# Kernel optimization log

Hardware: AMD Instinct MI355X
Metric: run time of the kernel (lower is better)

## Reference

```python
import jax, jax.numpy as jnp
import numpy as np

N = 100000   # nodes
E = 1600000  # edges (avg degree 16)
F_IN, F_HID, F_OUT = 128, 64, 16


def setup_inputs() -> dict:
    key = jax.random.key(0)
    ks = jax.random.split(key, 8)
    x = jax.random.normal(ks[0], (N, F_IN), jnp.float32)
    edge_index = jax.random.randint(ks[1], (2, E), 0, N, dtype=jnp.int32)
    def glorot(k, fan_in, fan_out):
        return jax.random.normal(k, (fan_in, fan_out), jnp.float32) * (1.0 / np.sqrt(fan_in))
    return {
        "x": x,
        "edge_index": edge_index,
        "W1": glorot(ks[2], F_IN, F_HID), "b1": jnp.zeros((F_HID,), jnp.float32),
        "W2": glorot(ks[3], F_HID, F_HID), "b2": jnp.zeros((F_HID,), jnp.float32),
        "W3": glorot(ks[4], F_HID, F_HID), "b3": jnp.zeros((F_HID,), jnp.float32),
        "W4": glorot(ks[5], F_HID, F_OUT), "b4": jnp.zeros((F_OUT,), jnp.float32),
    }


def _gcn_norm(edge_index, num_nodes):
    # Add self-loops and compute symmetric normalization D^-1/2 (A+I) D^-1/2
    loop = jnp.arange(num_nodes, dtype=edge_index.dtype)
    src = jnp.concatenate([edge_index[0], loop])
    dst = jnp.concatenate([edge_index[1], loop])
    deg = jax.ops.segment_sum(jnp.ones_like(dst, jnp.float32), dst, num_segments=num_nodes)
    dinv = jnp.where(deg > 0, jax.lax.rsqrt(deg), 0.0)
    norm = dinv[src] * dinv[dst]  # [E+N]
    return src, dst, norm


def _gcn_conv(x, W, b, src, dst, norm, num_nodes):
    h = x @ W                       # [N, F_out] small GEMM first (PyG order)
    msg = h[src] * norm[:, None]    # [E+N, F_out] gather + scale
    out = jax.ops.segment_sum(msg, dst, num_segments=num_nodes)
    return out + b


def reference(x, edge_index, W1, b1, W2, b2, W3, b3, W4, b4):
    src, dst, norm = _gcn_norm(edge_index, N)
    h = jax.nn.relu(_gcn_conv(x, W1, b1, src, dst, norm, N))  # dropout is identity in eval
    h = jax.nn.relu(_gcn_conv(h, W2, b2, src, dst, norm, N))
    h = jax.nn.relu(_gcn_conv(h, W3, b3, src, dst, norm, N))
    return _gcn_conv(h, W4, b4, src, dst, norm, N)
```

## Files before the change

kernel.cpp:

```cpp
#include <hip/hip_runtime.h>
#include <hip/hip_bf16.h>
#include <stdint.h>


#define TPB 256
#define MAXDEG 64
#define NGRP 8
#define NBLK_P 256
#define SLABCAP 1536
#define OVCAP 65536

typedef unsigned int uint;
typedef _Float16 h8 __attribute__((ext_vector_type(8)));
typedef _Float16 h16 __attribute__((ext_vector_type(16)));
typedef float f4 __attribute__((ext_vector_type(4)));

__device__ __forceinline__ int swz(int f) {
    return ((f >> 3) & 3) * 16 + (f >> 5) * 8 + (f & 7);
}

__device__ __forceinline__ int grp_of(int d, int chunk, float invchunk) {
    int g = (int)((float)d * invchunk);
    if (d >= (g + 1) * chunk) ++g;
    else if (d < g * chunk) --g;
    return g;
}

__global__ __launch_bounds__(TPB) void k_part(const int* __restrict__ src,
                                              const int* __restrict__ dst,
                                              uint* __restrict__ pcount,
                                              uint* __restrict__ ovcnt,
                                              int* __restrict__ ovbuf,
                                              uint* __restrict__ slab,
                                              int E, int chunk, float invchunk,
                                              int range) {
    __shared__ uint lcnt[NGRP];
    if (threadIdx.x < NGRP) lcnt[threadIdx.x] = 0;
    __syncthreads();
    const int e0 = blockIdx.x * range;
    const int e1 = (e0 + range < E) ? e0 + range : E;
    for (int e = e0 + (int)threadIdx.x; e < e1; e += TPB) {
        int d = dst[e];
        int s = src[e];
        int g = grp_of(d, chunk, invchunk);
        uint pos = atomicAdd(&lcnt[g], 1u);
        uint val = ((uint)(d - g * chunk) << 17) | (uint)s;
        if (pos < SLABCAP) {
            slab[((size_t)blockIdx.x * NGRP + g) * SLABCAP + pos] = val;
        } else {
            uint p = atomicAdd(ovcnt, 1u);
            if (p < OVCAP) { ovbuf[2 * p] = d; ovbuf[2 * p + 1] = s; }
        }
    }
    __syncthreads();
    if (threadIdx.x < NGRP) {
        uint c = lcnt[threadIdx.x];
        pcount[blockIdx.x * NGRP + threadIdx.x] = (c < SLABCAP) ? c : SLABCAP;
    }
}

__global__ __launch_bounds__(TPB) void k_fill(const uint* __restrict__ slab,
                                              const uint* __restrict__ pcount,
                                              const uint* __restrict__ ovcnt,
                                              const int* __restrict__ ovbuf,
                                              uint* __restrict__ cnt,
                                              int* __restrict__ bucket,
                                              int chunk) {
    const int grp = blockIdx.x & (NGRP - 1);
    const int blk = blockIdx.x >> 3;
    const int n = (int)pcount[blk * NGRP + grp];
    const uint* s = slab + ((size_t)blk * NGRP + grp) * SLABCAP;
    const int dbase = grp * chunk;
    int e = (int)threadIdx.x;
    for (; e + TPB < n; e += 2 * TPB) {
        uint v0 = s[e];
        uint v1 = s[e + TPB];
        int d0 = dbase + (int)(v0 >> 17), s0 = (int)(v0 & 0x1FFFFu);
        int d1 = dbase + (int)(v1 >> 17), s1 = (int)(v1 & 0x1FFFFu);
        uint p0 = atomicAdd(&cnt[d0], 1u);
        uint p1 = atomicAdd(&cnt[d1], 1u);
        if (p0 < MAXDEG) bucket[(size_t)d0 * MAXDEG + (int)p0] = s0;
        if (p1 < MAXDEG) bucket[(size_t)d1 * MAXDEG + (int)p1] = s1;
    }
    if (e < n) {
        uint v = s[e];
        int d = dbase + (int)(v >> 17), sv = (int)(v & 0x1FFFFu);
        uint p = atomicAdd(&cnt[d], 1u);
        if (p < MAXDEG) bucket[(size_t)d * MAXDEG + (int)p] = sv;
    }
    if (blk == 0) {
        uint on = *ovcnt;
        if (on > OVCAP) on = OVCAP;
        for (uint i = threadIdx.x; i < on; i += TPB) {
            int d = ovbuf[2 * i];
            if (d >= dbase && d < dbase + chunk) {
                int sv = ovbuf[2 * i + 1];
                uint p = atomicAdd(&cnt[d], 1u);
                if (p < MAXDEG) bucket[(size_t)d * MAXDEG + (int)p] = sv;
            }
        }
    }
}

__global__ __launch_bounds__(TPB) void k_gemm_mfma128(const float* __restrict__ X,
                                                      const float* __restrict__ W,
                                                      const uint* __restrict__ cnt,
                                                      _Float16* __restrict__ H,
                                                      int ngrp16, int nwaves, int n) {
    const int lane = threadIdx.x & 63;
    const int wid = blockIdx.x * (TPB / 64) + (threadIdx.x >> 6);
    const int nrow = lane & 15;
    const int kgrp = lane >> 4;

    h8 Bf[4][4];
#pragma unroll
    for (int kb = 0; kb < 4; ++kb)
#pragma unroll
        for (int j = 0; j < 8; ++j) {
            int k = kb * 32 + kgrp * 8 + j;
#pragma unroll
            for (int cb = 0; cb < 4; ++cb)
                Bf[kb][cb][j] = (_Float16)W[k * 64 + cb * 16 + nrow];
        }

    for (int g = wid; g < ngrp16; g += nwaves) {
        const int base = g * 16;
        int arow = base + nrow; if (arow >= n) arow = n - 1;
        const float* xr = X + (size_t)arow * 128;
        h8 A[4];
#pragma unroll
        for (int kb = 0; kb < 4; ++kb) {
            f4 lo = *(const f4*)(xr + kb * 32 + kgrp * 8);
            f4 hi = *(const f4*)(xr + kb * 32 + kgrp * 8 + 4);
#pragma unroll
            for (int j = 0; j < 4; ++j) { A[kb][j] = (_Float16)lo[j]; A[kb][4 + j] = (_Float16)hi[j]; }
        }
        f4 D[4];
#pragma unroll
        for (int cb = 0; cb < 4; ++cb) {
            f4 d = {0.f, 0.f, 0.f, 0.f};
#pragma unroll
            for (int kb = 0; kb < 4; ++kb)
                d = __builtin_amdgcn_mfma_f32_16x16x32_f16(A[kb], Bf[kb][cb], d, 0, 0, 0);
            D[cb] = d;
        }
#pragma unroll
        for (int r = 0; r < 4; ++r) {
            int onode = base + kgrp * 4 + r;
            if (onode < n) {
                float dio = rsqrtf((float)cnt[onode] + 1.0f);
#pragma unroll
                for (int cb = 0; cb < 4; ++cb)
                    H[(size_t)onode * 64 + swz(cb * 16 + nrow)] = (_Float16)(D[cb][r] * dio);
            }
        }
    }
}

template <int FOUT>
__global__ __launch_bounds__(TPB, 2) void k_agg_mfma(const _Float16* __restrict__ H,
                                                     const int* __restrict__ bucket,
                                                     const uint* __restrict__ cnt,
                                                     const float* __restrict__ b,
                                                     const float* __restrict__ W,
                                                     _Float16* __restrict__ Hout,
                                                     int ngrp16, int nwaves) {
    const int lane = threadIdx.x & 63;
    const int wid = blockIdx.x * (TPB / 64) + (threadIdx.x >> 6);
    const int nrow = lane & 15;
    const int kgrp = lane >> 4;
    const int kofs = kgrp * 16;
    constexpr int NCB = FOUT / 16;

    h8 Bf[2][NCB];
    float bias[16];
#pragma unroll
    for (int kb = 0; kb < 2; ++kb)
#pragma unroll
        for (int j = 0; j < 8; ++j) {
            int f = kb * 32 + kgrp * 8 + j;
            bias[kb * 8 + j] = b[f];
#pragma unroll
            for (int cb = 0; cb < NCB; ++cb)
                Bf[kb][cb][j] = (_Float16)W[f * FOUT + cb * 16 + nrow];
        }

    for (int g = wid; g < ngrp16; g += nwaves) {
        const int base = g * 16;
        const int node = base + nrow;
        const int cc = (int)cnt[node];
        const int cn = (cc < MAXDEG) ? cc : MAXDEG;

        float acc[16];
        {
            h16 sv = *(const h16*)(H + (size_t)node * 64 + kofs);
#pragma unroll
            for (int j = 0; j < 16; ++j) acc[j] = (float)sv[j];
        }
        const int* eb = bucket + (size_t)node * MAXDEG;
        int t = 0;
        for (; t + 4 <= cn; t += 4) {
            int i0 = eb[t], i1 = eb[t + 1], i2 = eb[t + 2], i3 = eb[t + 3];
            h16 v0 = *(const h16*)(H + (size_t)i0 * 64 + kofs);
            h16 v1 = *(const h16*)(H + (size_t)i1 * 64 + kofs);
            h16 v2 = *(const h16*)(H + (size_t)i2 * 64 + kofs);
            h16 v3 = *(const h16*)(H + (size_t)i3 * 64 + kofs);
#pragma unroll
            for (int j = 0; j < 16; ++j)
                acc[j] += ((float)v0[j] + (float)v1[j]) + ((float)v2[j] + (float)v3[j]);
        }
        if (t + 2 <= cn) {
            int i0 = eb[t], i1 = eb[t + 1];
            h16 v0 = *(const h16*)(H + (size_t)i0 * 64 + kofs);
            h16 v1 = *(const h16*)(H + (size_t)i1 * 64 + kofs);
#pragma unroll
            for (int j = 0; j < 16; ++j) acc[j] += (float)v0[j] + (float)v1[j];
            t += 2;
        }
        if (t < cn) {
            h16 v0 = *(const h16*)(H + (size_t)eb[t] * 64 + kofs);
#pragma unroll
            for (int j = 0; j < 16; ++j) acc[j] += (float)v0[j];
        }

        float di = rsqrtf((float)cc + 1.0f);
        h8 A0, A1;
#pragma unroll
        for (int j = 0; j < 8; ++j) {
            A0[j] = (_Float16)fmaxf(fmaf(di, acc[j], bias[j]), 0.f);
            A1[j] = (_Float16)fmaxf(fmaf(di, acc[8 + j], bias[8 + j]), 0.f);
        }

        f4 D[NCB];
#pragma unroll
        for (int cb = 0; cb < NCB; ++cb) {
            f4 d = {0.f, 0.f, 0.f, 0.f};
            d = __builtin_amdgcn_mfma_f32_16x16x32_f16(A0, Bf[0][cb], d, 0, 0, 0);
            d = __builtin_amdgcn_mfma_f32_16x16x32_f16(A1, Bf[1][cb], d, 0, 0, 0);
            D[cb] = d;
        }
#pragma unroll
        for (int r = 0; r < 4; ++r) {
            int onode = base + kgrp * 4 + r;
            float dio = rsqrtf((float)cnt[onode] + 1.0f);
#pragma unroll
            for (int cb = 0; cb < NCB; ++cb) {
                int f = cb * 16 + nrow;
                int p = (FOUT == 64) ? swz(f) : f;
                Hout[(size_t)onode * FOUT + p] = (_Float16)(D[cb][r] * dio);
            }
        }
    }
}

__global__ __launch_bounds__(TPB) void k_agg16(const _Float16* __restrict__ H,
                                               const int* __restrict__ bucket,
                                               const uint* __restrict__ cnt,
                                               const float* __restrict__ b,
                                               float* __restrict__ Out, int n) {
    int tid = blockIdx.x * TPB + threadIdx.x;
    int node = tid >> 4;
    int feat = tid & 15;
    if (node >= n) return;
    float s0 = (float)H[(size_t)node * 16 + feat];
    float s1 = 0.f, s2 = 0.f, s3 = 0.f, s4 = 0.f, s5 = 0.f, s6 = 0.f, s7 = 0.f;
    const int craw = (int)cnt[node];
    const int cn = (craw < MAXDEG) ? craw : MAXDEG;
    const int* eb = bucket + (size_t)node * MAXDEG;
    int t = 0;
    for (; t + 8 <= cn; t += 8) {
        int i0 = eb[t],     i1 = eb[t + 1], i2 = eb[t + 2], i3 = eb[t + 3];
        int i4 = eb[t + 4], i5 = eb[t + 5], i6 = eb[t + 6], i7 = eb[t + 7];
        float v0 = (float)H[(size_t)i0 * 16 + feat];
        float v1 = (float)H[(size_t)i1 * 16 + feat];
        float v2 = (float)H[(size_t)i2 * 16 + feat];
        float v3 = (float)H[(size_t)i3 * 16 + feat];
        float v4 = (float)H[(size_t)i4 * 16 + feat];
        float v5 = (float)H[(size_t)i5 * 16 + feat];
        float v6 = (float)H[(size_t)i6 * 16 + feat];
        float v7 = (float)H[(size_t)i7 * 16 + feat];
        s0 += v0; s1 += v1; s2 += v2; s3 += v3;
        s4 += v4; s5 += v5; s6 += v6; s7 += v7;
    }
    if (t + 4 <= cn) {
        int i0 = eb[t], i1 = eb[t + 1], i2 = eb[t + 2], i3 = eb[t + 3];
        s0 += (float)H[(size_t)i0 * 16 + feat];
        s1 += (float)H[(size_t)i1 * 16 + feat];
        s2 += (float)H[(size_t)i2 * 16 + feat];
        s3 += (float)H[(size_t)i3 * 16 + feat];
        t += 4;
    }
    if (t + 2 <= cn) {
        int i0 = eb[t], i1 = eb[t + 1];
        s0 += (float)H[(size_t)i0 * 16 + feat];
        s1 += (float)H[(size_t)i1 * 16 + feat];
        t += 2;
    }
    if (t < cn) s0 += (float)H[(size_t)eb[t] * 16 + feat];
    float di = rsqrtf((float)craw + 1.0f);
    float s = ((s0 + s1) + (s2 + s3)) + ((s4 + s5) + (s6 + s7));
    Out[(size_t)node * 16 + feat] = di * s + b[feat];
}

static inline size_t align256(size_t x) { return (x + 255) & ~(size_t)255; }

extern "C" void kernel_launch(void* const* d_in, const int* in_sizes, int n_in,
                              void* d_out, int out_size, void* d_ws, size_t ws_size,
                              hipStream_t stream) {
    const float* x  = (const float*)d_in[0];
    const int* ei   = (const int*)d_in[1];
    const float* W1 = (const float*)d_in[2];
    const float* b1 = (const float*)d_in[3];
    const float* W2 = (const float*)d_in[4];
    const float* b2 = (const float*)d_in[5];
    const float* W3 = (const float*)d_in[6];
    const float* b3 = (const float*)d_in[7];
    const float* W4 = (const float*)d_in[8];
    const float* b4 = (const float*)d_in[9];
    float* out = (float*)d_out;

    const int N = in_sizes[0] / 128;
    const int E = in_sizes[1] / 2;
    const int* src = ei;
    const int* dst = ei + E;

    const int chunk = (N + NGRP - 1) / NGRP;
    const float invchunk = 1.0f / (float)chunk;
    const int range = (E + NBLK_P - 1) / NBLK_P;

    char* p = (char*)d_ws;
    size_t off = 0;
    uint* cnt = (uint*)(p + off); off += align256((size_t)N * 4);
    uint* pcount = (uint*)(p + off); off += align256((size_t)NBLK_P * NGRP * 4);
    uint* ovcnt = (uint*)(p + off); off += 256;
    size_t zero_bytes = off;
    int* bucket = (int*)(p + off); off += align256((size_t)N * MAXDEG * 4);
    int* ovbuf = (int*)(p + off); off += align256((size_t)OVCAP * 8);
    _Float16* hA = (_Float16*)(p + off); off += align256((size_t)N * 64 * 2);
    _Float16* hB = (_Float16*)(p + off); off += align256((size_t)N * 64 * 2);
    uint* slab = (uint*)hB;
    (void)ws_size;

    hipMemsetAsync(d_ws, 0, zero_bytes, stream);

    k_part<<<NBLK_P, TPB, 0, stream>>>(src, dst, pcount, ovcnt, ovbuf, slab,
                                       E, chunk, invchunk, range);
    k_fill<<<NBLK_P * NGRP, TPB, 0, stream>>>(slab, pcount, ovcnt, ovbuf,
                                              cnt, bucket, chunk);

    const int ngrp16 = (N + 15) / 16;
    const int NBLK_M = (ngrp16 + (TPB / 64) - 1) / (TPB / 64);
    const int NWAVES_M = NBLK_M * (TPB / 64);

    k_gemm_mfma128<<<NBLK_M, TPB, 0, stream>>>(x, W1, cnt, hA, ngrp16, NWAVES_M, N);
    k_agg_mfma<64><<<NBLK_M, TPB, 0, stream>>>(hA, bucket, cnt, b1, W2, hB, ngrp16, NWAVES_M);
    k_agg_mfma<64><<<NBLK_M, TPB, 0, stream>>>(hB, bucket, cnt, b2, W3, hA, ngrp16, NWAVES_M);
    k_agg_mfma<16><<<NBLK_M, TPB, 0, stream>>>(hA, bucket, cnt, b3, W4, hB, ngrp16, NWAVES_M);
    int gAgg16 = (N * 16 + TPB - 1) / TPB;
    k_agg16<<<gAgg16, TPB, 0, stream>>>(hB, bucket, cnt, b4, out, N);
}
```

Before: 248.7 us.

## Replace global-atomic bucket fill with per-block LDS-counted destination subranges

The bucket-fill kernel now gives each block a subrange of destination nodes. Each block scans every partition slab for its group and counts slot positions with LDS atomics instead of global atomics on cnt. Counts are written to global memory once at the end, so cnt no longer has to be zeroed, and the memset now covers only the overflow counter. In exchange, each block reads all slab data for its group (32x redundant reads) and the launch shrinks to 256 blocks.

Result: slower. 370.4 us (+49.0%).

```diff
diff --git a/kernel.cpp b/kernel.cpp
--- a/kernel.cpp
+++ b/kernel.cpp
@@ -9,6 +9,7 @@
 #define NBLK_P 256
 #define SLABCAP 1536
 #define OVCAP 65536
+#define SUBR 32
 
 typedef unsigned int uint;
 typedef _Float16 h8 __attribute__((ext_vector_type(8)));
@@ -59,46 +60,70 @@
     }
 }
 
-__global__ __launch_bounds__(TPB) void k_fill(const uint* __restrict__ slab,
+__global__ __launch_bounds__(TPB) void k_sort(const uint* __restrict__ slab,
                                               const uint* __restrict__ pcount,
                                               const uint* __restrict__ ovcnt,
                                               const int* __restrict__ ovbuf,
                                               uint* __restrict__ cnt,
                                               int* __restrict__ bucket,
-                                              int chunk) {
+                                              int chunk, int n) {
+    __shared__ uint lcnt[(12500 + SUBR - 1) / SUBR + 8];
+    __shared__ uint pcs[NBLK_P];
     const int grp = blockIdx.x & (NGRP - 1);
-    const int blk = blockIdx.x >> 3;
-    const int n = (int)pcount[blk * NGRP + grp];
-    const uint* s = slab + ((size_t)blk * NGRP + grp) * SLABCAP;
-    const int dbase = grp * chunk;
-    int e = (int)threadIdx.x;
-    for (; e + TPB < n; e += 2 * TPB) {
-        uint v0 = s[e];
-        uint v1 = s[e + TPB];
-        int d0 = dbase + (int)(v0 >> 17), s0 = (int)(v0 & 0x1FFFFu);
-        int d1 = dbase + (int)(v1 >> 17), s1 = (int)(v1 & 0x1FFFFu);
-        uint p0 = atomicAdd(&cnt[d0], 1u);
-        uint p1 = atomicAdd(&cnt[d1], 1u);
-        if (p0 < MAXDEG) bucket[(size_t)d0 * MAXDEG + (int)p0] = s0;
-        if (p1 < MAXDEG) bucket[(size_t)d1 * MAXDEG + (int)p1] = s1;
-    }
-    if (e < n) {
-        uint v = s[e];
-        int d = dbase + (int)(v >> 17), sv = (int)(v & 0x1FFFFu);
-        uint p = atomicAdd(&cnt[d], 1u);
-        if (p < MAXDEG) bucket[(size_t)d * MAXDEG + (int)p] = sv;
-    }
-    if (blk == 0) {
+    const int sub = blockIdx.x >> 3;
+    const int span = (chunk + SUBR - 1) / SUBR;
+    const int nlo = sub * span;
+    int nhi = nlo + span; if (nhi > chunk) nhi = chunk;
+    const int nspan = nhi - nlo;
+    for (int i = threadIdx.x; i < nspan; i += TPB) lcnt[i] = 0;
+    for (int i = threadIdx.x; i < NBLK_P; i += TPB) pcs[i] = pcount[i * NGRP + grp];
+    __syncthreads();
+    const int dgbase = grp * chunk;
+    for (int blk = 0; blk < NBLK_P; ++blk) {
+        const int nn = (int)pcs[blk];
+        const uint* s = slab + ((size_t)blk * NGRP + grp) * SLABCAP;
+        const uint4* s4 = (const uint4*)s;
+        const int nq = nn >> 2;
+        for (int q = (int)threadIdx.x; q < nq; q += TPB) {
+            uint4 v4 = s4[q];
+            uint vv[4] = {v4.x, v4.y, v4.z, v4.w};
+#pragma unroll
+            for (int u = 0; u < 4; ++u) {
+                int dl = (int)(vv[u] >> 17);
+                if (dl >= nlo && dl < nhi) {
+                    uint pos = atomicAdd(&lcnt[dl - nlo], 1u);
+                    if (pos < MAXDEG)
+                        bucket[(size_t)(dgbase + dl) * MAXDEG + (int)pos] = (int)(vv[u] & 0x1FFFFu);
+                }
+            }
+        }
+        for (int e = (nq << 2) + (int)threadIdx.x; e < nn; e += TPB) {
+            uint v = s[e];
+            int dl = (int)(v >> 17);
+            if (dl >= nlo && dl < nhi) {
+                uint pos = atomicAdd(&lcnt[dl - nlo], 1u);
+                if (pos < MAXDEG)
+                    bucket[(size_t)(dgbase + dl) * MAXDEG + (int)pos] = (int)(v & 0x1FFFFu);
+            }
+        }
+    }
+    {
         uint on = *ovcnt;
         if (on > OVCAP) on = OVCAP;
         for (uint i = threadIdx.x; i < on; i += TPB) {
             int d = ovbuf[2 * i];
-            if (d >= dbase && d < dbase + chunk) {
-                int sv = ovbuf[2 * i + 1];
-                uint p = atomicAdd(&cnt[d], 1u);
-                if (p < MAXDEG) bucket[(size_t)d * MAXDEG + (int)p] = sv;
-            }
-        }
+            int dl = d - dgbase;
+            if (dl >= nlo && dl < nhi) {
+                uint pos = atomicAdd(&lcnt[dl - nlo], 1u);
+                if (pos < MAXDEG)
+                    bucket[(size_t)d * MAXDEG + (int)pos] = ovbuf[2 * i + 1];
+            }
+        }
+    }
+    __syncthreads();
+    for (int i = threadIdx.x; i < nspan; i += TPB) {
+        int node = dgbase + nlo + i;
+        if (node < n) cnt[node] = lcnt[i];
     }
 }
 
@@ -330,10 +355,10 @@
 
     char* p = (char*)d_ws;
     size_t off = 0;
+    uint* ovcnt = (uint*)(p + off); off += 256;
+    size_t zero_bytes = off;
     uint* cnt = (uint*)(p + off); off += align256((size_t)N * 4);
     uint* pcount = (uint*)(p + off); off += align256((size_t)NBLK_P * NGRP * 4);
-    uint* ovcnt = (uint*)(p + off); off += 256;
-    size_t zero_bytes = off;
     int* bucket = (int*)(p + off); off += align256((size_t)N * MAXDEG * 4);
     int* ovbuf = (int*)(p + off); off += align256((size_t)OVCAP * 8);
     _Float16* hA = (_Float16*)(p + off); off += align256((size_t)N * 64 * 2);
@@ -345,8 +370,8 @@
 
     k_part<<<NBLK_P, TPB, 0, stream>>>(src, dst, pcount, ovcnt, ovbuf, slab,
                                        E, chunk, invchunk, range);
-    k_fill<<<NBLK_P * NGRP, TPB, 0, stream>>>(slab, pcount, ovcnt, ovbuf,
-                                              cnt, bucket, chunk);
+    k_sort<<<NGRP * SUBR, TPB, 0, stream>>>(slab, pcount, ovcnt, ovbuf,
+                                            cnt, bucket, chunk, N);
 
     const int ngrp16 = (N + 15) / 16;
     const int NBLK_M = (ngrp16 + (TPB / 64) - 1) / (TPB / 64);
```

## Bin edges into fine node spans and build buckets with shared-memory atomics

Applied to the files above, without the earlier changes.

Edge partitioning now bins destinations into 256 fine node spans instead of 8 coarse groups. The fill kernel is replaced by a per-span sort kernel that counts degrees with shared-memory atomics and writes the final counts once, replacing global atomics on the count array. The count and partition-count arrays no longer need zeroing, and the slab buffer moves to hA so it can span both feature buffers. In exchange, k_part scatters its writes across many more small slabs, and each sort thread serially walks one slab with strided, poorly coalesced reads. Every sort block also rescans the whole overflow buffer.

After: 203.6 us. -18.2%, faster.

```diff
diff --git a/kernel.cpp b/kernel.cpp
--- a/kernel.cpp
+++ b/kernel.cpp
@@ -5,9 +5,9 @@
 
 #define TPB 256
 #define MAXDEG 64
-#define NGRP 8
+#define NFG 256
 #define NBLK_P 256
-#define SLABCAP 1536
+#define SCAP 96
 #define OVCAP 65536
 
 typedef unsigned int uint;
@@ -19,10 +19,10 @@
     return ((f >> 3) & 3) * 16 + (f >> 5) * 8 + (f & 7);
 }
 
-__device__ __forceinline__ int grp_of(int d, int chunk, float invchunk) {
-    int g = (int)((float)d * invchunk);
-    if (d >= (g + 1) * chunk) ++g;
-    else if (d < g * chunk) --g;
+__device__ __forceinline__ int grp_of(int d, int span, float invspan) {
+    int g = (int)((float)d * invspan);
+    if (d >= (g + 1) * span) ++g;
+    else if (d < g * span) --g;
     return g;
 }
 
@@ -32,74 +32,74 @@
                                               uint* __restrict__ ovcnt,
                                               int* __restrict__ ovbuf,
                                               uint* __restrict__ slab,
-                                              int E, int chunk, float invchunk,
+                                              int E, int span, float invspan,
                                               int range) {
-    __shared__ uint lcnt[NGRP];
-    if (threadIdx.x < NGRP) lcnt[threadIdx.x] = 0;
+    __shared__ uint lcnt[NFG];
+    for (int i = threadIdx.x; i < NFG; i += TPB) lcnt[i] = 0;
     __syncthreads();
     const int e0 = blockIdx.x * range;
     const int e1 = (e0 + range < E) ? e0 + range : E;
     for (int e = e0 + (int)threadIdx.x; e < e1; e += TPB) {
         int d = dst[e];
         int s = src[e];
-        int g = grp_of(d, chunk, invchunk);
-        uint pos = atomicAdd(&lcnt[g], 1u);
-        uint val = ((uint)(d - g * chunk) << 17) | (uint)s;
-        if (pos < SLABCAP) {
-            slab[((size_t)blockIdx.x * NGRP + g) * SLABCAP + pos] = val;
+        int fg = grp_of(d, span, invspan);
+        uint pos = atomicAdd(&lcnt[fg], 1u);
+        uint val = ((uint)(d - fg * span) << 17) | (uint)s;
+        if (pos < SCAP) {
+            slab[((size_t)blockIdx.x * NFG + fg) * SCAP + pos] = val;
         } else {
             uint p = atomicAdd(ovcnt, 1u);
             if (p < OVCAP) { ovbuf[2 * p] = d; ovbuf[2 * p + 1] = s; }
         }
     }
     __syncthreads();
-    if (threadIdx.x < NGRP) {
-        uint c = lcnt[threadIdx.x];
-        pcount[blockIdx.x * NGRP + threadIdx.x] = (c < SLABCAP) ? c : SLABCAP;
-    }
-}
-
-__global__ __launch_bounds__(TPB) void k_fill(const uint* __restrict__ slab,
+    for (int i = threadIdx.x; i < NFG; i += TPB) {
+        uint c = lcnt[i];
+        pcount[(size_t)i * NBLK_P + blockIdx.x] = (c < SCAP) ? c : SCAP;
+    }
+}
+
+__global__ __launch_bounds__(TPB) void k_sort(const uint* __restrict__ slab,
                                               const uint* __restrict__ pcount,
                                               const uint* __restrict__ ovcnt,
                                               const int* __restrict__ ovbuf,
                                               uint* __restrict__ cnt,
                                               int* __restrict__ bucket,
-                                              int chunk) {
-    const int grp = blockIdx.x & (NGRP - 1);
-    const int blk = blockIdx.x >> 3;
-    const int n = (int)pcount[blk * NGRP + grp];
-    const uint* s = slab + ((size_t)blk * NGRP + grp) * SLABCAP;
-    const int dbase = grp * chunk;
-    int e = (int)threadIdx.x;
-    for (; e + TPB < n; e += 2 * TPB) {
-        uint v0 = s[e];
-        uint v1 = s[e + TPB];
-        int d0 = dbase + (int)(v0 >> 17), s0 = (int)(v0 & 0x1FFFFu);
-        int d1 = dbase + (int)(v1 >> 17), s1 = (int)(v1 & 0x1FFFFu);
-        uint p0 = atomicAdd(&cnt[d0], 1u);
-        uint p1 = atomicAdd(&cnt[d1], 1u);
-        if (p0 < MAXDEG) bucket[(size_t)d0 * MAXDEG + (int)p0] = s0;
-        if (p1 < MAXDEG) bucket[(size_t)d1 * MAXDEG + (int)p1] = s1;
-    }
-    if (e < n) {
-        uint v = s[e];
-        int d = dbase + (int)(v >> 17), sv = (int)(v & 0x1FFFFu);
-        uint p = atomicAdd(&cnt[d], 1u);
-        if (p < MAXDEG) bucket[(size_t)d * MAXDEG + (int)p] = sv;
-    }
-    if (blk == 0) {
+                                              int span, int n) {
+    __shared__ uint lcnt[512];
+    const int fg = blockIdx.x;
+    const int nlo = fg * span;
+    int nspan = span;
+    if (nlo + nspan > n) nspan = (n > nlo) ? (n - nlo) : 0;
+    for (int i = threadIdx.x; i < span; i += TPB) lcnt[i] = 0;
+    __syncthreads();
+    {
+        const int t = (int)threadIdx.x;
+        const uint nn = pcount[(size_t)fg * NBLK_P + t];
+        const uint* s = slab + ((size_t)t * NFG + fg) * SCAP;
+        for (uint i = 0; i < nn; ++i) {
+            uint v = s[i];
+            int dl = (int)(v >> 17);
+            uint pos = atomicAdd(&lcnt[dl], 1u);
+            if (pos < MAXDEG)
+                bucket[(size_t)(nlo + dl) * MAXDEG + (int)pos] = (int)(v & 0x1FFFFu);
+        }
+    }
+    {
         uint on = *ovcnt;
         if (on > OVCAP) on = OVCAP;
         for (uint i = threadIdx.x; i < on; i += TPB) {
             int d = ovbuf[2 * i];
-            if (d >= dbase && d < dbase + chunk) {
-                int sv = ovbuf[2 * i + 1];
-                uint p = atomicAdd(&cnt[d], 1u);
-                if (p < MAXDEG) bucket[(size_t)d * MAXDEG + (int)p] = sv;
+            int dl = d - nlo;
+            if (dl >= 0 && dl < nspan) {
+                uint pos = atomicAdd(&lcnt[dl], 1u);
+                if (pos < MAXDEG)
+                    bucket[(size_t)d * MAXDEG + (int)pos] = ovbuf[2 * i + 1];
             }
         }
     }
+    __syncthreads();
+    for (int i = threadIdx.x; i < nspan; i += TPB) cnt[nlo + i] = lcnt[i];
 }
 
 __global__ __launch_bounds__(TPB) void k_gemm_mfma128(const float* __restrict__ X,
@@ -324,29 +324,29 @@
     const int* src = ei;
     const int* dst = ei + E;
 
-    const int chunk = (N + NGRP - 1) / NGRP;
-    const float invchunk = 1.0f / (float)chunk;
+    const int span = (N + NFG - 1) / NFG;
+    const float invspan = 1.0f / (float)span;
     const int range = (E + NBLK_P - 1) / NBLK_P;
 
     char* p = (char*)d_ws;
     size_t off = 0;
-    uint* cnt = (uint*)(p + off); off += align256((size_t)N * 4);
-    uint* pcount = (uint*)(p + off); off += align256((size_t)NBLK_P * NGRP * 4);
     uint* ovcnt = (uint*)(p + off); off += 256;
     size_t zero_bytes = off;
+    uint* cnt = (uint*)(p + off); off += align256((size_t)N * 4);
+    uint* pcount = (uint*)(p + off); off += align256((size_t)NFG * NBLK_P * 4);
     int* bucket = (int*)(p + off); off += align256((size_t)N * MAXDEG * 4);
     int* ovbuf = (int*)(p + off); off += align256((size_t)OVCAP * 8);
     _Float16* hA = (_Float16*)(p + off); off += align256((size_t)N * 64 * 2);
     _Float16* hB = (_Float16*)(p + off); off += align256((size_t)N * 64 * 2);
-    uint* slab = (uint*)hB;
+    uint* slab = (uint*)hA;
     (void)ws_size;
 
     hipMemsetAsync(d_ws, 0, zero_bytes, stream);
 
     k_part<<<NBLK_P, TPB, 0, stream>>>(src, dst, pcount, ovcnt, ovbuf, slab,
-                                       E, chunk, invchunk, range);
-    k_fill<<<NBLK_P * NGRP, TPB, 0, stream>>>(slab, pcount, ovcnt, ovbuf,
-                                              cnt, bucket, chunk);
+                                       E, span, invspan, range);
+    k_sort<<<NFG, TPB, 0, stream>>>(slab, pcount, ovcnt, ovbuf,
+                                    cnt, bucket, span, N);
 
     const int ngrp16 = (N + 15) / 16;
     const int NBLK_M = (ngrp16 + (TPB / 64) - 1) / (TPB / 64);
```
